# Optimization experiments

Hardware: AMD Instinct MI355X
Metric: run time of the kernel (lower is better)

## Reference

```python
import jax, jax.numpy as jnp
import numpy as np

RADIUS = 0.1
NSAMPLE = 64
NEVENT = 2048
B, N, D = 4, 16384, 62
CHANNEL = D + 2  # 64


def index_events(events, idx):
    # events: [B, N, C], idx: [B, ...] -> [B, ..., C]
    return jax.vmap(lambda e, i: e[i])(events, idx)


def square_distance(src, dst):
    # src: [B, S, 2], dst: [B, N, 2] -> [B, S, N]
    return (jnp.sum(src ** 2, -1)[:, :, None]
            + jnp.sum(dst ** 2, -1)[:, None, :]
            - 2.0 * jnp.einsum('bsc,bnc->bsn', src, dst))


def research_circle(radius, nsample, xy, new_xy):
    n = xy.shape[1]
    sqrdists = square_distance(new_xy, xy)            # [B, S, N]
    ar = jnp.arange(n, dtype=jnp.int32)
    group_idx = jnp.where(sqrdists > radius ** 2, n, ar)  # out-of-ball -> N (sorts last)
    group_idx = jnp.sort(group_idx, axis=-1)[:, :, :nsample]
    first = group_idx[:, :, :1]
    return jnp.where(group_idx == n, first, group_idx)     # [B, S, nsample]


def reference(xy, events, fps_idx, affine_alpha, affine_beta):
    b, _, c = xy.shape
    new_xy = index_events(xy, fps_idx)                     # [B, S, 2]
    idx = research_circle(RADIUS, NSAMPLE, xy, new_xy)     # [B, S, K]
    grouped_xy = index_events(xy, idx)                     # [B, S, K, 2]
    grouped_events = index_events(events, idx)             # [B, S, K, D]
    # Normalize (normalize='center')
    g = jnp.concatenate([grouped_events, grouped_xy], axis=-1)  # [B, S, K, D+2]
    mean = jnp.mean(g, axis=2, keepdims=True)              # [B, S, 1, C]
    centered = g - mean
    std = jnp.std(centered.reshape(b, -1), axis=-1, ddof=1)[:, None, None, None]
    g = centered / (std + 1e-05)
    new_events = affine_alpha * g + affine_beta            # [B, S, K, 64]
    return new_xy, new_events


def setup_inputs() -> dict:
    key = jax.random.key(0)
    k1, k2, k3 = jax.random.split(key, 3)
    xy = jax.random.uniform(k1, (B, N, 2), dtype=jnp.float32)
    events = jax.random.normal(k2, (B, N, D), dtype=jnp.float32)
    fps_idx = jax.random.randint(k3, (B, NEVENT), 0, N, dtype=jnp.int32)
    affine_alpha = jnp.ones((1, 1, 1, CHANNEL), dtype=jnp.float32)
    affine_beta = jnp.zeros((1, 1, 1, CHANNEL), dtype=jnp.float32)
    return {"xy": xy, "events": events, "fps_idx": fps_idx,
            "affine_alpha": affine_alpha, "affine_beta": affine_beta}
```

## Files before the change

### kernel.cpp

```cpp
#include <hip/hip_runtime.h>
#include <stdint.h>
#include <math.h>

#define NPTS 16384
#define DEV 62
#define NEVENT 2048
#define NSAMPLE 64
#define CH 64
#define NBATCH 4
#define STOT (NBATCH * NEVENT)
#define M_PER_BATCH (NEVENT * NSAMPLE * CH)

#define OUT1_BASE 16384
#define REG_STRIDE (NSAMPLE * CH)
#define WS_MEAN 0
#define WS_SS   (STOT * CH)

__device__ __forceinline__ int swz_query8192(int blk) {
    int x = blk & 7;
    int j = blk >> 3;
    return (x & 3) * NEVENT + (x >> 2) * (NEVENT / 2) + j;
}
__device__ __forceinline__ int swz_group2048(int blk) {
    int x = blk & 7;
    int j = blk >> 3;
    return (x & 3) * (NEVENT / 4) + (x >> 2) * (NEVENT / 8) + j;
}

__global__ __launch_bounds__(256) void knn_stats_kernel(
    const float2* __restrict__ xy,
    const float* __restrict__ ev,
    const int* __restrict__ fps,
    float* __restrict__ ws,
    float* __restrict__ out)
{
    int grp  = swz_group2048(blockIdx.x);
    int w    = threadIdx.x >> 6;
    int lane = threadIdx.x & 63;
    int wave = grp * 4 + w;
    int b    = grp >> 9;

    __shared__ int   sidx[4][NSAMPLE];
    __shared__ float ssum[2][256];
    __shared__ float smean[CH];
    __shared__ float swred[4];

    const float2* xyb = xy + b * NPTS;
    int qi = fps[wave];
    float2 q = xyb[qi];
    if (lane == 0) ((float2*)out)[wave] = q;

    float ssq = __fadd_rn(__fmul_rn(q.x, q.x), __fmul_rn(q.y, q.y));
    const float thr = 0.01f;

    int* regidx = (int*)(out + OUT1_BASE + (size_t)wave * REG_STRIDE);
    int m = 0;
    int first = -1;

    for (int base = 0; base < NPTS; base += 256) {
        float2 p0 = xyb[base       + lane];
        float2 p1 = xyb[base +  64 + lane];
        float2 p2 = xyb[base + 128 + lane];
        float2 p3 = xyb[base + 192 + lane];

        auto proc = [&](float2 p, int idxbase) {
            float ssp = __fadd_rn(__fmul_rn(p.x, p.x), __fmul_rn(p.y, p.y));
            float dot = __builtin_fmaf(q.y, p.y, __fmul_rn(q.x, p.x));
            float d   = __fsub_rn(__fadd_rn(ssq, ssp), __fmul_rn(2.0f, dot));
            bool ok = !(d > thr);
            unsigned long long bal = __ballot(ok);
            if (first < 0 && bal != 0ull)
                first = idxbase + (__ffsll((unsigned long long)bal) - 1);
            if (ok) {
                int pos = m + __popcll(bal & ((1ull << lane) - 1ull));
                if (pos < NSAMPLE) {
                    regidx[pos]  = idxbase + lane;
                    sidx[w][pos] = idxbase + lane;
                }
            }
            m += __popcll(bal);
        };
        proc(p0, base);
        proc(p1, base + 64);
        proc(p2, base + 128);
        proc(p3, base + 192);
        if (m >= NSAMPLE) break;
    }
    if (m < NSAMPLE) {
        for (int p = m + lane; p < NSAMPLE; p += 64) {
            regidx[p]  = first;
            sidx[w][p] = first;
        }
    }

    __syncthreads();

    int tid = threadIdx.x;
    int c2 = tid & 31;
    int kq = tid >> 5;
    const float* evb = ev + (size_t)b * NPTS * DEV;

    for (int qq = 0; qq < 4; ++qq) {
        int s = grp * 4 + qq;

        float g0[8], g1[8];
        float a0 = 0.f, a1 = 0.f;
#pragma unroll
        for (int j = 0; j < 8; ++j) {
            int row = sidx[qq][8 * j + kq];
            float2 v;
            if (c2 < 31) v = *(const float2*)(evb + (size_t)row * DEV + 2 * c2);
            else         v = xyb[row];
            g0[j] = v.x; g1[j] = v.y;
            a0 += v.x;   a1 += v.y;
        }
        ssum[0][tid] = a0;
        ssum[1][tid] = a1;
        __syncthreads();

        if (tid < CH) {
            int which = tid >> 5, cc = tid & 31;
            float t = 0.f;
#pragma unroll
            for (int p = 0; p < 8; ++p) t += ssum[which][p * 32 + cc];
            smean[2 * cc + which] = t * (1.0f / NSAMPLE);
        }
        __syncthreads();

        if (tid < CH) ws[WS_MEAN + (size_t)s * CH + tid] = smean[tid];

        float m0 = smean[2 * c2], m1 = smean[2 * c2 + 1];
        float ss = 0.f;
#pragma unroll
        for (int j = 0; j < 8; ++j) {
            float c0 = g0[j] - m0;
            float c1 = g1[j] - m1;
            ss += c0 * c0 + c1 * c1;
        }

        for (int off = 32; off > 0; off >>= 1) ss += __shfl_down(ss, off, 64);
        if ((tid & 63) == 0) swred[tid >> 6] = ss;
        __syncthreads();
        if (tid == 0) ws[WS_SS + s] = swred[0] + swred[1] + swred[2] + swred[3];
        __syncthreads();
    }
}

__global__ __launch_bounds__(256) void finalize_kernel(
    const float2* __restrict__ xy,
    const float* __restrict__ ev,
    const float* __restrict__ alpha,
    const float* __restrict__ beta,
    const float* __restrict__ ws,
    float* __restrict__ out)
{
    int s = swz_query8192(blockIdx.x);
    int b = s >> 11;
    int tid = threadIdx.x;
    float* reg = out + OUT1_BASE + (size_t)s * REG_STRIDE;

    __shared__ int sidx[NSAMPLE];
    __shared__ float sm[CH], sa[CH], sbet[CH];
    __shared__ double sd[256];
    __shared__ float sinv;

    if (tid < NSAMPLE) {
        sidx[tid] = ((const int*)reg)[tid];
        sm[tid]   = ws[WS_MEAN + (size_t)s * CH + tid];
    } else if (tid < 128) {
        sa[tid - 64]   = alpha[tid - 64];
        sbet[tid - 64] = beta[tid - 64];
    }

    double acc = 0.0;
    for (int i = tid; i < NEVENT; i += 256)
        acc += (double)ws[WS_SS + b * NEVENT + i];
    sd[tid] = acc;
    __syncthreads();
    for (int off = 128; off > 0; off >>= 1) {
        if (tid < off) sd[tid] += sd[tid + off];
        __syncthreads();
    }
    if (tid == 0) {
        double stdv = sqrt(sd[0] / (double)(M_PER_BATCH - 1));
        sinv = (float)(1.0 / (stdv + 1e-5));
    }
    __syncthreads();

    int c2 = tid & 31;
    int kq = tid >> 5;
    float inv = sinv;

    const float* evb = ev + (size_t)b * NPTS * DEV;
    const float2* xyb = xy + b * NPTS;

    float m0 = sm[2 * c2],   m1 = sm[2 * c2 + 1];
    float al0 = sa[2 * c2],  al1 = sa[2 * c2 + 1];
    float be0 = sbet[2 * c2], be1 = sbet[2 * c2 + 1];

    float2* outp = (float2*)reg;
#pragma unroll
    for (int j = 0; j < 8; ++j) {
        int row = sidx[8 * j + kq];
        float2 v;
        if (c2 < 31) v = *(const float2*)(evb + (size_t)row * DEV + 2 * c2);
        else         v = xyb[row];
        float2 r;
        r.x = al0 * ((v.x - m0) * inv) + be0;
        r.y = al1 * ((v.y - m1) * inv) + be1;
        float* pp = (float*)&outp[256 * j + tid];
        __builtin_nontemporal_store(r.x, pp);
        __builtin_nontemporal_store(r.y, pp + 1);
    }
}

extern "C" void kernel_launch(void* const* d_in, const int* in_sizes, int n_in,
                              void* d_out, int out_size, void* d_ws, size_t ws_size,
                              hipStream_t stream) {
    const float2* xy    = (const float2*)d_in[0];
    const float*  ev    = (const float*)d_in[1];
    const int*    fps   = (const int*)d_in[2];
    const float*  alpha = (const float*)d_in[3];
    const float*  beta  = (const float*)d_in[4];
    float* out = (float*)d_out;
    float* ws  = (float*)d_ws;

    knn_stats_kernel<<<STOT / 4, 256, 0, stream>>>(xy, ev, fps, ws, out);
    finalize_kernel<<<STOT, 256, 0, stream>>>(xy, ev, alpha, beta, ws, out);
}
```

Measured before the change: 196.3 us.

## Bucket query points spatially so neighboring waves gather nearby event rows

Adds a per-batch kernel that bins the FPS query points into a 16x16 spatial grid and builds a permutation sorted by cell. Both the kNN/stats and finalize kernels now map blocks through this permutation, so concurrently running blocks handle spatially close queries whose gathered event rows overlap, improving L2/MALL reuse. This replaces the old fixed block swizzle. It also switches the nontemporal output stores to plain float2 stores. The cost is an extra tiny launch and one indirection load per block.

```diff
diff --git a/kernel.cpp b/kernel.cpp
--- a/kernel.cpp
+++ b/kernel.cpp
@@ -13,37 +13,79 @@
 
 #define OUT1_BASE 16384
 #define REG_STRIDE (NSAMPLE * CH)
-#define WS_MEAN 0
-#define WS_SS   (STOT * CH)
-
-__device__ __forceinline__ int swz_query8192(int blk) {
-    int x = blk & 7;
-    int j = blk >> 3;
-    return (x & 3) * NEVENT + (x >> 2) * (NEVENT / 2) + j;
-}
-__device__ __forceinline__ int swz_group2048(int blk) {
-    int x = blk & 7;
-    int j = blk >> 3;
-    return (x & 3) * (NEVENT / 4) + (x >> 2) * (NEVENT / 8) + j;
-}
+#define WS_PERM 0
+#define WS_MEAN STOT
+#define WS_SS   (WS_MEAN + STOT * CH)
+
+__global__ __launch_bounds__(256) void bucket_kernel(
+    const float2* __restrict__ xy,
+    const int* __restrict__ fps,
+    int* __restrict__ perm)
+{
+    int b = blockIdx.x;
+    int tid = threadIdx.x;
+    __shared__ int   hist[256];
+    __shared__ int   offs[256];
+    __shared__ short skey[NEVENT];
+
+    hist[tid] = 0;
+    __syncthreads();
+
+    const float2* xyb = xy + b * NPTS;
+    const int* fpsb = fps + b * NEVENT;
+    for (int i = tid; i < NEVENT; i += 256) {
+        float2 q = xyb[fpsb[i]];
+        int cx = (int)(q.x * 16.0f); cx = cx < 0 ? 0 : (cx > 15 ? 15 : cx);
+        int cy = (int)(q.y * 16.0f); cy = cy < 0 ? 0 : (cy > 15 ? 15 : cy);
+        int key = cy * 16 + cx;
+        skey[i] = (short)key;
+        atomicAdd(&hist[key], 1);
+    }
+    __syncthreads();
+
+    int v = hist[tid];
+    offs[tid] = v;
+    __syncthreads();
+    for (int d = 1; d < 256; d <<= 1) {
+        int t = (tid >= d) ? offs[tid - d] : 0;
+        __syncthreads();
+        offs[tid] += t;
+        __syncthreads();
+    }
+    hist[tid] = offs[tid] - v;
+    __syncthreads();
+
+    for (int i = tid; i < NEVENT; i += 256) {
+        int pos = atomicAdd(&hist[(int)skey[i]], 1);
+        perm[b * NEVENT + pos] = i;
+    }
+}
+
 
 __global__ __launch_bounds__(256) void knn_stats_kernel(
     const float2* __restrict__ xy,
     const float* __restrict__ ev,
     const int* __restrict__ fps,
+    const int* __restrict__ perm,
     float* __restrict__ ws,
     float* __restrict__ out)
 {
-    int grp  = swz_group2048(blockIdx.x);
+    int x    = blockIdx.x & 7;
+    int b    = x & 3;
+    int half = x >> 2;
+    int j    = blockIdx.x >> 3;
     int w    = threadIdx.x >> 6;
     int lane = threadIdx.x & 63;
-    int wave = grp * 4 + w;
-    int b    = grp >> 9;
+    int p    = half * 1024 + 4 * j + w;
+    int wave = b * NEVENT + perm[b * NEVENT + p];
 
     __shared__ int   sidx[4][NSAMPLE];
+    __shared__ int   sqid[4];
     __shared__ float ssum[2][256];
     __shared__ float smean[CH];
     __shared__ float swred[4];
+
+    if (lane == 0) sqid[w] = wave;
 
     const float2* xyb = xy + b * NPTS;
     int qi = fps[wave];
@@ -63,9 +105,9 @@
         float2 p2 = xyb[base + 128 + lane];
         float2 p3 = xyb[base + 192 + lane];
 
-        auto proc = [&](float2 p, int idxbase) {
-            float ssp = __fadd_rn(__fmul_rn(p.x, p.x), __fmul_rn(p.y, p.y));
-            float dot = __builtin_fmaf(q.y, p.y, __fmul_rn(q.x, p.x));
+        auto proc = [&](float2 pt, int idxbase) {
+            float ssp = __fadd_rn(__fmul_rn(pt.x, pt.x), __fmul_rn(pt.y, pt.y));
+            float dot = __builtin_fmaf(q.y, pt.y, __fmul_rn(q.x, pt.x));
             float d   = __fsub_rn(__fadd_rn(ssq, ssp), __fmul_rn(2.0f, dot));
             bool ok = !(d > thr);
             unsigned long long bal = __ballot(ok);
@@ -87,9 +129,9 @@
         if (m >= NSAMPLE) break;
     }
     if (m < NSAMPLE) {
-        for (int p = m + lane; p < NSAMPLE; p += 64) {
-            regidx[p]  = first;
-            sidx[w][p] = first;
+        for (int pfill = m + lane; pfill < NSAMPLE; pfill += 64) {
+            regidx[pfill]  = first;
+            sidx[w][pfill] = first;
         }
     }
 
@@ -101,18 +143,18 @@
     const float* evb = ev + (size_t)b * NPTS * DEV;
 
     for (int qq = 0; qq < 4; ++qq) {
-        int s = grp * 4 + qq;
+        int s = sqid[qq];
 
         float g0[8], g1[8];
         float a0 = 0.f, a1 = 0.f;
 #pragma unroll
-        for (int j = 0; j < 8; ++j) {
-            int row = sidx[qq][8 * j + kq];
+        for (int jj = 0; jj < 8; ++jj) {
+            int row = sidx[qq][8 * jj + kq];
             float2 v;
             if (c2 < 31) v = *(const float2*)(evb + (size_t)row * DEV + 2 * c2);
             else         v = xyb[row];
-            g0[j] = v.x; g1[j] = v.y;
-            a0 += v.x;   a1 += v.y;
+            g0[jj] = v.x; g1[jj] = v.y;
+            a0 += v.x;    a1 += v.y;
         }
         ssum[0][tid] = a0;
         ssum[1][tid] = a1;
@@ -122,7 +164,7 @@
             int which = tid >> 5, cc = tid & 31;
             float t = 0.f;
 #pragma unroll
-            for (int p = 0; p < 8; ++p) t += ssum[which][p * 32 + cc];
+            for (int pq = 0; pq < 8; ++pq) t += ssum[which][pq * 32 + cc];
             smean[2 * cc + which] = t * (1.0f / NSAMPLE);
         }
         __syncthreads();
@@ -132,9 +174,9 @@
         float m0 = smean[2 * c2], m1 = smean[2 * c2 + 1];
         float ss = 0.f;
 #pragma unroll
-        for (int j = 0; j < 8; ++j) {
-            float c0 = g0[j] - m0;
-            float c1 = g1[j] - m1;
+        for (int jj = 0; jj < 8; ++jj) {
+            float c0 = g0[jj] - m0;
+            float c1 = g1[jj] - m1;
             ss += c0 * c0 + c1 * c1;
         }
 
@@ -151,11 +193,16 @@
     const float* __restrict__ ev,
     const float* __restrict__ alpha,
     const float* __restrict__ beta,
+    const int* __restrict__ perm,
     const float* __restrict__ ws,
     float* __restrict__ out)
 {
-    int s = swz_query8192(blockIdx.x);
-    int b = s >> 11;
+    int x    = blockIdx.x & 7;
+    int b    = x & 3;
+    int half = x >> 2;
+    int j    = blockIdx.x >> 3;
+    int p    = half * 1024 + j;
+    int s    = b * NEVENT + perm[b * NEVENT + p];
     int tid = threadIdx.x;
     float* reg = out + OUT1_BASE + (size_t)s * REG_STRIDE;
 
@@ -200,17 +247,15 @@
 
     float2* outp = (float2*)reg;
 #pragma unroll
-    for (int j = 0; j < 8; ++j) {
-        int row = sidx[8 * j + kq];
+    for (int jj = 0; jj < 8; ++jj) {
+        int row = sidx[8 * jj + kq];
         float2 v;
         if (c2 < 31) v = *(const float2*)(evb + (size_t)row * DEV + 2 * c2);
         else         v = xyb[row];
         float2 r;
         r.x = al0 * ((v.x - m0) * inv) + be0;
         r.y = al1 * ((v.y - m1) * inv) + be1;
-        float* pp = (float*)&outp[256 * j + tid];
-        __builtin_nontemporal_store(r.x, pp);
-        __builtin_nontemporal_store(r.y, pp + 1);
+        outp[256 * jj + tid] = r;
     }
 }
 
@@ -224,7 +269,9 @@
     const float*  beta  = (const float*)d_in[4];
     float* out = (float*)d_out;
     float* ws  = (float*)d_ws;
-
-    knn_stats_kernel<<<STOT / 4, 256, 0, stream>>>(xy, ev, fps, ws, out);
-    finalize_kernel<<<STOT, 256, 0, stream>>>(xy, ev, alpha, beta, ws, out);
-}
+    int*   perm = (int*)ws;
+
+    bucket_kernel<<<NBATCH, 256, 0, stream>>>(xy, fps, perm);
+    knn_stats_kernel<<<STOT / 4, 256, 0, stream>>>(xy, ev, fps, perm, ws, out);
+    finalize_kernel<<<STOT, 256, 0, stream>>>(xy, ev, alpha, beta, perm, ws, out);
+}
```

After: 201.8 us. 2.8% more time.
